# Kernel optimization log

Measured on AMD Instinct MI355X. Metric: run time of the kernel, lower is better.

The kernel has to match this reference:

```python
import jax, jax.numpy as jnp
import numpy as np

N, D = 2048, 64
H, W = 128, 128
NEAR, RADIUS_CLIP, BLUR = 0.01, 3.0, 0.3
A_MIN, A_MAX = 1.0 / 255.0, 0.999


def setup_inputs():
    key = jax.random.key(0)
    k = jax.random.split(key, 6)
    xy = jax.random.uniform(k[0], (N, 2), minval=-1.2, maxval=1.2)
    zz = jax.random.uniform(k[1], (N, 1), minval=3.0, maxval=5.0)
    means = jnp.concatenate([xy, zz], axis=1).astype(jnp.float32)
    quats = jax.random.normal(k[2], (N, 4), dtype=jnp.float32)
    scales = jax.random.normal(k[3], (N, 3), dtype=jnp.float32) * 0.3 - 2.2  # log-scales
    opacities = jax.random.normal(k[4], (N,), dtype=jnp.float32) * 0.5 + 1.0  # logits
    gs_features = jax.random.normal(k[5], (N, D), dtype=jnp.float32) * 0.5
    c2o = jnp.eye(4, dtype=jnp.float32)
    K = jnp.array([[200.0, 0.0, 64.0], [0.0, 200.0, 64.0], [0.0, 0.0, 1.0]], dtype=jnp.float32)
    return dict(means=means, quats=quats, scales=scales, opacities=opacities,
                gs_features=gs_features, c2o=c2o, K=K, width=W, height=H)


def _quat_to_rot(q):
    q = q / jnp.linalg.norm(q, axis=-1, keepdims=True)
    w, x, y, z = q[:, 0], q[:, 1], q[:, 2], q[:, 3]
    r0 = jnp.stack([1 - 2 * (y * y + z * z), 2 * (x * y - w * z), 2 * (x * z + w * y)], -1)
    r1 = jnp.stack([2 * (x * y + w * z), 1 - 2 * (x * x + z * z), 2 * (y * z - w * x)], -1)
    r2 = jnp.stack([2 * (x * z - w * y), 2 * (y * z + w * x), 1 - 2 * (x * x + y * y)], -1)
    return jnp.stack([r0, r1, r2], -2)  # [N,3,3]


def _rasterize(means, quats, log_scales, opac_logits, colors, viewmat, K, width, height):
    Rv, tv = viewmat[:3, :3], viewmat[:3, 3]
    fx, fy, cx, cy = K[0, 0], K[1, 1], K[0, 2], K[1, 2]
    mc = means @ Rv.T + tv                      # camera-space means [N,3]
    x, y, z = mc[:, 0], mc[:, 1], mc[:, 2]
    # 3D covariance Sigma = R S S^T R^T, rotated into camera frame
    M = _quat_to_rot(quats) * jnp.exp(log_scales)[:, None, :]
    cov_w = M @ jnp.swapaxes(M, 1, 2)           # [N,3,3]
    cov_c = jnp.einsum('ij,njk,lk->nil', Rv, cov_w, Rv)
    # perspective (EWA) Jacobian [N,2,3]
    rz = 1.0 / z
    zero = jnp.zeros_like(z)
    J = jnp.stack([jnp.stack([fx * rz, zero, -fx * x * rz * rz], -1),
                   jnp.stack([zero, fy * rz, -fy * y * rz * rz], -1)], -2)
    cov2d = jnp.einsum('nij,njk,nlk->nil', J, cov_c, J)
    a = cov2d[:, 0, 0] + BLUR
    b = cov2d[:, 0, 1]
    c = cov2d[:, 1, 1] + BLUR
    det = a * c - b * b
    cA, cB, cC = c / det, -b / det, a / det     # conic = inverse 2D covariance
    mx = fx * x * rz + cx
    my = fy * y * rz + cy
    # cull: behind near plane, degenerate, or projected 3-sigma radius below radius_clip
    lam_max = 0.5 * (a + c) + jnp.sqrt(jnp.maximum(0.25 * (a - c) ** 2 + b * b, 1e-12))
    radius = 3.0 * jnp.sqrt(lam_max)
    valid = (z > NEAR) & (det > 0) & (radius > RADIUS_CLIP)
    opac = jax.nn.sigmoid(opac_logits)
    # global front-to-back depth order (single camera)
    order = jnp.argsort(z)
    mx, my, cA, cB, cC = mx[order], my[order], cA[order], cB[order], cC[order]
    opac, valid, colors = opac[order], valid[order], colors[order]
    # per pixel-gaussian evaluation, [H,W,N]
    px = jnp.arange(width, dtype=means.dtype) + 0.5
    py = jnp.arange(height, dtype=means.dtype) + 0.5
    dx = px[None, :, None] - mx[None, None, :]
    dy = py[:, None, None] - my[None, None, :]
    sigma = 0.5 * (cA * dx * dx + cC * dy * dy) + cB * dx * dy
    alpha = jnp.minimum(opac * jnp.exp(-sigma), A_MAX)
    alpha = jnp.where((sigma >= 0) & valid & (alpha >= A_MIN), alpha, 0.0)
    # front-to-back alpha compositing: exclusive transmittance cumprod
    Tcum = jnp.cumprod(1.0 - alpha, axis=-1)
    T_excl = jnp.concatenate([jnp.ones_like(Tcum[..., :1]), Tcum[..., :-1]], axis=-1)
    out = jnp.einsum('hwn,nd->hwd', alpha * T_excl, colors)
    return out[None]  # [1,H,W,D]


def reference(means, quats, scales, opacities, gs_features, c2o, K, width, height):
    viewmat = jnp.linalg.inv(c2o)
    return _rasterize(means, quats, scales, opacities, gs_features, viewmat, K, width, height)
```

## Files before the change

kernel.cpp:

```cpp
#include <hip/hip_runtime.h>

constexpr int NG  = 2048;
constexpr int DF  = 64;
constexpr int IW  = 128;
constexpr int IH  = 128;

#define P_NEAR 0.01f
#define P_BLUR 0.3f
#define P_AMIN (1.0f/255.0f)
#define P_AMAX 0.999f

__device__ inline void invert4x4(const float* m, float* inv) {
    inv[0]  =  m[5]*m[10]*m[15] - m[5]*m[11]*m[14] - m[9]*m[6]*m[15] + m[9]*m[7]*m[14] + m[13]*m[6]*m[11] - m[13]*m[7]*m[10];
    inv[4]  = -m[4]*m[10]*m[15] + m[4]*m[11]*m[14] + m[8]*m[6]*m[15] - m[8]*m[7]*m[14] - m[12]*m[6]*m[11] + m[12]*m[7]*m[10];
    inv[8]  =  m[4]*m[9]*m[15]  - m[4]*m[11]*m[13] - m[8]*m[5]*m[15] + m[8]*m[7]*m[13] + m[12]*m[5]*m[11] - m[12]*m[7]*m[9];
    inv[12] = -m[4]*m[9]*m[14]  + m[4]*m[10]*m[13] + m[8]*m[5]*m[14] - m[8]*m[6]*m[13] - m[12]*m[5]*m[10] + m[12]*m[6]*m[9];
    inv[1]  = -m[1]*m[10]*m[15] + m[1]*m[11]*m[14] + m[9]*m[2]*m[15] - m[9]*m[3]*m[14] - m[13]*m[2]*m[11] + m[13]*m[3]*m[10];
    inv[5]  =  m[0]*m[10]*m[15] - m[0]*m[11]*m[14] - m[8]*m[2]*m[15] + m[8]*m[3]*m[14] + m[12]*m[2]*m[11] - m[12]*m[3]*m[10];
    inv[9]  = -m[0]*m[9]*m[15]  + m[0]*m[11]*m[13] + m[8]*m[1]*m[15] - m[8]*m[3]*m[13] - m[12]*m[1]*m[11] + m[12]*m[3]*m[9];
    inv[13] =  m[0]*m[9]*m[14]  - m[0]*m[10]*m[13] - m[8]*m[1]*m[14] + m[8]*m[2]*m[13] + m[12]*m[1]*m[10] - m[12]*m[2]*m[9];
    inv[2]  =  m[1]*m[6]*m[15]  - m[1]*m[7]*m[14]  - m[5]*m[2]*m[15] + m[5]*m[3]*m[14] + m[13]*m[2]*m[7]  - m[13]*m[3]*m[6];
    inv[6]  = -m[0]*m[6]*m[15]  + m[0]*m[7]*m[14]  + m[4]*m[2]*m[15] - m[4]*m[3]*m[14] - m[12]*m[2]*m[7]  + m[12]*m[3]*m[6];
    inv[10] =  m[0]*m[5]*m[15]  - m[0]*m[7]*m[13]  - m[4]*m[1]*m[15] + m[4]*m[3]*m[13] + m[12]*m[1]*m[7]  - m[12]*m[3]*m[5];
    inv[14] = -m[0]*m[5]*m[14]  + m[0]*m[6]*m[13]  + m[4]*m[1]*m[14] - m[4]*m[2]*m[13] - m[12]*m[1]*m[6]  + m[12]*m[2]*m[5];
    inv[3]  = -m[1]*m[6]*m[11]  + m[1]*m[7]*m[10]  + m[5]*m[2]*m[11] - m[5]*m[3]*m[10] - m[9]*m[2]*m[7]   + m[9]*m[3]*m[6];
    inv[7]  =  m[0]*m[6]*m[11]  - m[0]*m[7]*m[10]  - m[4]*m[2]*m[11] + m[4]*m[3]*m[10] + m[8]*m[2]*m[7]   - m[8]*m[3]*m[6];
    inv[11] = -m[0]*m[5]*m[11]  + m[0]*m[7]*m[9]   + m[4]*m[1]*m[11] - m[4]*m[3]*m[9]  - m[8]*m[1]*m[7]   + m[8]*m[3]*m[5];
    inv[15] =  m[0]*m[5]*m[10]  - m[0]*m[6]*m[9]   - m[4]*m[1]*m[10] + m[4]*m[2]*m[9]  + m[8]*m[1]*m[6]   - m[8]*m[2]*m[5];
    float det = m[0]*inv[0] + m[1]*inv[4] + m[2]*inv[8] + m[3]*inv[12];
    det = 1.0f / det;
    #pragma unroll
    for (int i = 0; i < 16; ++i) inv[i] *= det;
}

constexpr int NZ  = 8;
constexpr int RB  = 1024;
constexpr int CAP = 1024;

constexpr int L_T    = 0;
constexpr int L_CNT  = 512;
constexpr int L_SIDX = 528;
constexpr int L_OVL  = L_SIDX + CAP;
constexpr int L_PRM  = L_OVL;
constexpr int L_KEYS = L_PRM + CAP * 8;
constexpr int L_ACC  = L_OVL;
constexpr int ACC_ST = 66;
constexpr int L_TOTAL = L_OVL + NZ * 64 * ACC_ST;

__global__ __launch_bounds__(RB, 4) void fused_render_kernel(
    const float* __restrict__ means,  const float* __restrict__ quats,
    const float* __restrict__ scales, const float* __restrict__ opac_logits,
    const float* __restrict__ colors, const float* __restrict__ c2o,
    const float* __restrict__ Kmat,   float* __restrict__ out)
{
    extern __shared__ float lds[];
    int*                cnt  = (int*)(lds + L_CNT);
    int*                sidx = (int*)(lds + L_SIDX);
    unsigned long long* keys = (unsigned long long*)(lds + L_KEYS);
    float4*             prm4 = (float4*)(lds + L_PRM);

    const int tid  = threadIdx.x;
    const int lane = tid & 63;
    const int wv16 = tid >> 6;
    const int sz   = wv16 >> 1;
    const int hh   = wv16 & 1;
    const int tile = blockIdx.x;
    const int tx = (tile & 15) * 8;
    const int ty = (tile >> 4) * 8;
    const float px = tx + (lane & 7) + 0.5f;
    const float py = ty + (lane >> 3) + 0.5f;
    const float cxt = tx + 4.0f, cyt = ty + 4.0f;

    if (tid == 0) *cnt = 0;
    __syncthreads();

    {
        float inv[16];
        {
            float m[16];
            #pragma unroll
            for (int t = 0; t < 16; ++t) m[t] = c2o[t];
            invert4x4(m, inv);
        }
        const float fx = Kmat[0], fy = Kmat[4], cx = Kmat[2], cy = Kmat[5];

        #pragma unroll
        for (int c = 0; c < NG / RB; ++c) {
            const int g = c * RB + tid;
            float mx = means[g*3+0], my = means[g*3+1], mz = means[g*3+2];
            float X = inv[0]*mx + inv[1]*my + inv[2]*mz  + inv[3];
            float Y = inv[4]*mx + inv[5]*my + inv[6]*mz  + inv[7];
            float Z = inv[8]*mx + inv[9]*my + inv[10]*mz + inv[11];

            float qw = quats[g*4+0], qx = quats[g*4+1], qy = quats[g*4+2], qz = quats[g*4+3];
            float qn = rsqrtf(qw*qw + qx*qx + qy*qy + qz*qz);
            qw *= qn; qx *= qn; qy *= qn; qz *= qn;
            float R00 = 1.f - 2.f*(qy*qy + qz*qz), R01 = 2.f*(qx*qy - qw*qz), R02 = 2.f*(qx*qz + qw*qy);
            float R10 = 2.f*(qx*qy + qw*qz), R11 = 1.f - 2.f*(qx*qx + qz*qz), R12 = 2.f*(qy*qz - qw*qx);
            float R20 = 2.f*(qx*qz - qw*qy), R21 = 2.f*(qy*qz + qw*qx), R22 = 1.f - 2.f*(qx*qx + qy*qy);

            float s0 = expf(scales[g*3+0]), s1 = expf(scales[g*3+1]), s2 = expf(scales[g*3+2]);
            float M00 = R00*s0, M01 = R01*s1, M02 = R02*s2;
            float M10 = R10*s0, M11 = R11*s1, M12 = R12*s2;
            float M20 = R20*s0, M21 = R21*s1, M22 = R22*s2;

            float V00 = M00*M00 + M01*M01 + M02*M02;
            float V01 = M00*M10 + M01*M11 + M02*M12;
            float V02 = M00*M20 + M01*M21 + M02*M22;
            float V11 = M10*M10 + M11*M11 + M12*M12;
            float V12 = M10*M20 + M11*M21 + M12*M22;
            float V22 = M20*M20 + M21*M21 + M22*M22;

            float Rv[3][3] = {{inv[0],inv[1],inv[2]},{inv[4],inv[5],inv[6]},{inv[8],inv[9],inv[10]}};
            float Vm[3][3] = {{V00,V01,V02},{V01,V11,V12},{V02,V12,V22}};
            float Tm[3][3], C[3][3];
            #pragma unroll
            for (int r = 0; r < 3; ++r)
                #pragma unroll
                for (int cc = 0; cc < 3; ++cc)
                    Tm[r][cc] = Rv[r][0]*Vm[0][cc] + Rv[r][1]*Vm[1][cc] + Rv[r][2]*Vm[2][cc];
            #pragma unroll
            for (int r = 0; r < 3; ++r)
                #pragma unroll
                for (int cc = 0; cc < 3; ++cc)
                    C[r][cc] = Tm[r][0]*Rv[cc][0] + Tm[r][1]*Rv[cc][1] + Tm[r][2]*Rv[cc][2];

            float rz = 1.0f / Z;
            float j00 = fx*rz, j02 = -fx*X*rz*rz;
            float j11 = fy*rz, j12 = -fy*Y*rz*rz;

            float c00 = j00*j00*C[0][0] + 2.f*j00*j02*C[0][2] + j02*j02*C[2][2];
            float c01 = j00*j11*C[0][1] + j00*j12*C[0][2] + j02*j11*C[1][2] + j02*j12*C[2][2];
            float c11 = j11*j11*C[1][1] + 2.f*j11*j12*C[1][2] + j12*j12*C[2][2];

            float a = c00 + P_BLUR;
            float b = c01;
            float cc_ = c11 + P_BLUR;
            float det = a*cc_ - b*b;

            float pmx = fx*X*rz + cx;
            float pmy = fy*Y*rz + cy;

            float lam = 0.5f*(a + cc_) + sqrtf(fmaxf(0.25f*(a - cc_)*(a - cc_) + b*b, 1e-12f));
            float radius = 3.0f * sqrtf(lam);
            bool valid = (Z > P_NEAR) && (det > 0.0f) && (radius > 3.0f);

            float op = 1.0f / (1.0f + expf(-opac_logits[g]));

            bool sel = false;
            float cA = 0.f, cB = 0.f, cC2 = 0.f;
            if (valid) {
                float rdet = 1.0f / det;
                cA = cc_ * rdet; cB = -b * rdet; cC2 = a * rdet;
                float smax = logf(255.0f * op);
                if (smax > 0.f) {
                    float rx = sqrtf(2.f * a   * smax) * 1.0001f + 1e-3f;
                    float ry = sqrtf(2.f * cc_ * smax) * 1.0001f + 1e-3f;
                    sel = (fabsf(pmx - cxt) <= rx + 3.5f) && (fabsf(pmy - cyt) <= ry + 3.5f);
                }
            }

            unsigned long long m = __ballot(sel);
            int wbase = 0;
            if (lane == 0 && m) wbase = atomicAdd(cnt, (int)__popcll(m));
            wbase = __shfl(wbase, 0);
            if (sel) {
                int pos = wbase + (int)__popcll(m & ((1ull << lane) - 1ull));
                if (pos < CAP) {
                    prm4[pos*2]   = make_float4(pmx, pmy, cA, cB);
                    prm4[pos*2+1] = make_float4(cC2, op, __int_as_float(g), 0.f);
                    keys[pos] = ((unsigned long long)__float_as_uint(Z) << 32) | (unsigned)g;
                }
            }
        }
    }
    __syncthreads();
    int L = *cnt;
    if (L > CAP) L = CAP;

    {
        int padL = (L + 1) & ~1;
        if (tid < padL - L) keys[L + tid] = ~0ull;
        __syncthreads();
        const ulonglong2* k2 = (const ulonglong2*)keys;
        if (tid < L) {
            unsigned long long kk = keys[tid];
            int rank = 0;
            #pragma unroll 2
            for (int c = 0; c < padL / 2; ++c) {
                ulonglong2 q = k2[c];
                rank += (q.x < kk) + (q.y < kk);
            }
            sidx[rank] = tid;
        }
    }
    __syncthreads();

    float acc[32];
    #pragma unroll
    for (int f = 0; f < 32; ++f) acc[f] = 0.f;
    float T = 1.0f;

    {
        const int r0 = (sz * L) >> 3;
        const int r1 = ((sz + 1) * L) >> 3;
        const float4* cph = (const float4*)colors + hh * 8;
        if (r1 > r0) {
            int k = sidx[r0];
            float4 e0 = prm4[k*2], e1 = prm4[k*2+1];
            for (int r = r0; r < r1; ++r) {
                int kn = (r + 1 < r1) ? sidx[r + 1] : k;
                float4 n0 = prm4[kn*2], n1 = prm4[kn*2+1];

                float dx = px - e0.x, dy = py - e0.y;
                float sig = 0.5f*(e0.z*dx*dx + e1.x*dy*dy) + e0.w*dx*dy;
                float al = fminf(e1.y * __expf(-sig), P_AMAX);
                al = (sig >= 0.f && al >= P_AMIN) ? al : 0.f;

                if (__ballot(al > 0.f)) {
                    float wv = T * al;
                    const float4* crow = cph + (size_t)(unsigned)__float_as_int(e1.z) * 16;
                    #pragma unroll
                    for (int q = 0; q < 8; ++q) {
                        float4 cv = crow[q];
                        acc[4*q+0] = fmaf(wv, cv.x, acc[4*q+0]);
                        acc[4*q+1] = fmaf(wv, cv.y, acc[4*q+1]);
                        acc[4*q+2] = fmaf(wv, cv.z, acc[4*q+2]);
                        acc[4*q+3] = fmaf(wv, cv.w, acc[4*q+3]);
                    }
                    T *= (1.f - al);
                    if (!__ballot(T >= 1e-6f)) break;
                }
                e0 = n0; e1 = n1; k = kn;
            }
        }
    }

    if (hh == 0) lds[L_T + sz*64 + lane] = T;
    __syncthreads();
    {
        float* ab = lds + L_ACC + (size_t)(sz * 64 + lane) * ACC_ST + hh * 32;
        #pragma unroll
        for (int q = 0; q < 16; ++q)
            *(float2*)(ab + 2*q) = make_float2(acc[2*q], acc[2*q+1]);
    }
    __syncthreads();

    {
        int p  = tid >> 4;
        int f0 = (tid & 15) * 4;
        float r0, r1, r2, r3;
        const float* ab = lds + L_ACC + (size_t)((NZ-1)*64 + p) * ACC_ST + f0;
        { float2 u = *(const float2*)ab, v = *(const float2*)(ab + 2);
          r0 = u.x; r1 = u.y; r2 = v.x; r3 = v.y; }
        #pragma unroll
        for (int s = NZ - 2; s >= 0; --s) {
            float Ts = lds[L_T + s*64 + p];
            const float* as_ = lds + L_ACC + (size_t)(s*64 + p) * ACC_ST + f0;
            float2 u = *(const float2*)as_, v = *(const float2*)(as_ + 2);
            r0 = fmaf(Ts, r0, u.x); r1 = fmaf(Ts, r1, u.y);
            r2 = fmaf(Ts, r2, v.x); r3 = fmaf(Ts, r3, v.y);
        }
        int pyg = ty + (p >> 3), pxg = tx + (p & 7);
        float* op_ = out + (size_t)(pyg * IW + pxg) * DF + f0;
        *(float4*)op_ = make_float4(r0, r1, r2, r3);
    }
}

constexpr int ZSL    = 8;
constexpr int NSEG   = 2;
constexpr int NFB    = 2;
constexpr int RTH    = 512;
constexpr int NTILES = 256;
constexpr int EST    = 12;

constexpr size_t WS_SA   = 0;
constexpr size_t WS_SB   = WS_SA   + NG*4;
constexpr size_t WS_SC   = WS_SB   + NG*4;
constexpr size_t WS_SG   = WS_SC   + NG*4;
constexpr size_t WS_T0   = WS_SG   + NG;
constexpr size_t WS_ACC1 = WS_T0   + NTILES*64;
constexpr size_t WS_TCNT = WS_ACC1 + (size_t)NTILES*64*DF;
constexpr size_t WS_TPRM = WS_TCNT + NTILES;
constexpr size_t WS_TOTAL= WS_TPRM + (size_t)NTILES*CAP*8;

__global__ __launch_bounds__(512) void prep_sort_kernel(
    const float* __restrict__ means,  const float* __restrict__ quats,
    const float* __restrict__ scales, const float* __restrict__ opac_logits,
    const float* __restrict__ c2o,    const float* __restrict__ Kmat,
    float* __restrict__ ws)
{
    __shared__ __align__(16) unsigned zlds[NG];
    __shared__ int cnt[8][64];
    const int tid  = threadIdx.x;
    const int lane = tid & 63;
    const int part = tid >> 6;
    const int b    = blockIdx.x;
    const int gown = b * 64 + lane;

    float inv[16];
    {
        float m[16];
        #pragma unroll
        for (int t = 0; t < 16; ++t) m[t] = c2o[t];
        invert4x4(m, inv);
    }
    const float fx = Kmat[0], fy = Kmat[4], cx = Kmat[2], cy = Kmat[5];

    #pragma unroll
    for (int u = 0; u < NG/512; ++u) {
        const int g = u*512 + tid;
        float mx = means[g*3+0], my = means[g*3+1], mz = means[g*3+2];
        float Z = inv[8]*mx + inv[9]*my + inv[10]*mz + inv[11];
        zlds[g] = __float_as_uint(Z);
    }

    float4 A = make_float4(0.f,0.f,0.f,0.f);
    float4 B = make_float4(0.f,0.f,-1e9f,-1e9f);
    if (part == 0) {
        const int g = gown;
        float mx = means[g*3+0], my = means[g*3+1], mz = means[g*3+2];
        float X = inv[0]*mx + inv[1]*my + inv[2]*mz  + inv[3];
        float Y = inv[4]*mx + inv[5]*my + inv[6]*mz  + inv[7];
        float Z = inv[8]*mx + inv[9]*my + inv[10]*mz + inv[11];

        float qw = quats[g*4+0], qx = quats[g*4+1], qy = quats[g*4+2], qz = quats[g*4+3];
        float qn = rsqrtf(qw*qw + qx*qx + qy*qy + qz*qz);
        qw *= qn; qx *= qn; qy *= qn; qz *= qn;
        float R00 = 1.f - 2.f*(qy*qy + qz*qz), R01 = 2.f*(qx*qy - qw*qz), R02 = 2.f*(qx*qz + qw*qy);
        float R10 = 2.f*(qx*qy + qw*qz), R11 = 1.f - 2.f*(qx*qx + qz*qz), R12 = 2.f*(qy*qz - qw*qx);
        float R20 = 2.f*(qx*qz - qw*qy), R21 = 2.f*(qy*qz + qw*qx), R22 = 1.f - 2.f*(qx*qx + qy*qy);

        float s0 = expf(scales[g*3+0]), s1 = expf(scales[g*3+1]), s2 = expf(scales[g*3+2]);
        float M00 = R00*s0, M01 = R01*s1, M02 = R02*s2;
        float M10 = R10*s0, M11 = R11*s1, M12 = R12*s2;
        float M20 = R20*s0, M21 = R21*s1, M22 = R22*s2;

        float V00 = M00*M00 + M01*M01 + M02*M02;
        float V01 = M00*M10 + M01*M11 + M02*M12;
        float V02 = M00*M20 + M01*M21 + M02*M22;
        float V11 = M10*M10 + M11*M11 + M12*M12;
        float V12 = M10*M20 + M11*M21 + M12*M22;
        float V22 = M20*M20 + M21*M21 + M22*M22;

        float Rv[3][3] = {{inv[0],inv[1],inv[2]},{inv[4],inv[5],inv[6]},{inv[8],inv[9],inv[10]}};
        float Vm[3][3] = {{V00,V01,V02},{V01,V11,V12},{V02,V12,V22}};
        float Tm[3][3], C[3][3];
        #pragma unroll
        for (int r = 0; r < 3; ++r)
            #pragma unroll
            for (int cc = 0; cc < 3; ++cc)
                Tm[r][cc] = Rv[r][0]*Vm[0][cc] + Rv[r][1]*Vm[1][cc] + Rv[r][2]*Vm[2][cc];
        #pragma unroll
        for (int r = 0; r < 3; ++r)
            #pragma unroll
            for (int cc = 0; cc < 3; ++cc)
                C[r][cc] = Tm[r][0]*Rv[cc][0] + Tm[r][1]*Rv[cc][1] + Tm[r][2]*Rv[cc][2];

        float rz = 1.0f / Z;
        float j00 = fx*rz, j02 = -fx*X*rz*rz;
        float j11 = fy*rz, j12 = -fy*Y*rz*rz;

        float c00 = j00*j00*C[0][0] + 2.f*j00*j02*C[0][2] + j02*j02*C[2][2];
        float c01 = j00*j11*C[0][1] + j00*j12*C[0][2] + j02*j11*C[1][2] + j02*j12*C[2][2];
        float c11 = j11*j11*C[1][1] + 2.f*j11*j12*C[1][2] + j12*j12*C[2][2];

        float a = c00 + P_BLUR;
        float bb = c01;
        float cc_ = c11 + P_BLUR;
        float det = a*cc_ - bb*bb;

        float pmx = fx*X*rz + cx;
        float pmy = fy*Y*rz + cy;

        float lam = 0.5f*(a + cc_) + sqrtf(fmaxf(0.25f*(a - cc_)*(a - cc_) + bb*bb, 1e-12f));
        float radius = 3.0f * sqrtf(lam);
        bool valid = (Z > P_NEAR) && (det > 0.0f) && (radius > 3.0f);

        float op = 1.0f / (1.0f + expf(-opac_logits[g]));

        float cA = 0.f, cB = 0.f, cC2 = 0.f, rx = -1e9f, ry = -1e9f;
        if (valid) {
            float rdet = 1.0f / det;
            cA = cc_ * rdet; cB = -bb * rdet; cC2 = a * rdet;
            float smax = logf(255.0f * op);
            if (smax > 0.f) {
                rx = sqrtf(2.f * a   * smax) * 1.0001f + 1e-3f;
                ry = sqrtf(2.f * cc_ * smax) * 1.0001f + 1e-3f;
            }
        }
        A = make_float4(pmx, pmy, cA, cB);
        B = make_float4(cC2, op, rx, ry);
    }
    __syncthreads();

    const unsigned kk = zlds[b*64 + lane];
    const uint4* zl4 = (const uint4*)zlds;
    int c = 0;
    #pragma unroll 4
    for (int i = part*64; i < part*64 + 64; ++i) {
        uint4 q = zl4[i];
        const int j = i * 4;
        c += (q.x < kk || (q.x == kk && j+0 < gown)) ? 1 : 0;
        c += (q.y < kk || (q.y == kk && j+1 < gown)) ? 1 : 0;
        c += (q.z < kk || (q.z == kk && j+2 < gown)) ? 1 : 0;
        c += (q.w < kk || (q.w == kk && j+3 < gown)) ? 1 : 0;
    }
    cnt[part][lane] = c;
    __syncthreads();
    if (part == 0) {
        int rank = 0;
        #pragma unroll
        for (int e = 0; e < 8; ++e) rank += cnt[e][lane];
        ((float4*)(ws + WS_SA))[rank] = A;
        ((float4*)(ws + WS_SB))[rank] = B;
        ((float4*)(ws + WS_SC))[rank] = make_float4(A.x, A.y, B.z, B.w);
        ((int*)  (ws + WS_SG))[rank] = gown;
    }
}

__global__ __launch_bounds__(512) void cull_tile_kernel(float* __restrict__ ws)
{
    __shared__ int s_wcnt[8];
    const int tid  = threadIdx.x;
    const int lane = tid & 63;
    const int w    = tid >> 6;
    const int tile = blockIdx.x;
    const int tx = (tile & 15) * 8, ty = (tile >> 4) * 8;
    const float cxt = tx + 4.0f, cyt = ty + 4.0f;

    const float4* sA = (const float4*)(ws + WS_SA);
    const float4* sB = (const float4*)(ws + WS_SB);
    const float4* sC = (const float4*)(ws + WS_SC);
    const int*    sG = (const int*)  (ws + WS_SG);
    float4* tp = (float4*)(ws + WS_TPRM + (size_t)tile * CAP * 8);

    int Lrun = 0;
    #pragma unroll
    for (int ch = 0; ch < NG/RTH; ++ch) {
        const int j = ch*RTH + tid;
        float4 C = sC[j];
        bool sel = (fabsf(C.x - cxt) <= C.z + 3.5f) && (fabsf(C.y - cyt) <= C.w + 3.5f);
        unsigned long long m = __ballot(sel);
        if (lane == 0) s_wcnt[w] = (int)__popcll(m);
        __syncthreads();
        int pre = 0, tot = 0;
        #pragma unroll
        for (int e = 0; e < 8; ++e) { int cw = s_wcnt[e]; pre += (e < w) ? cw : 0; tot += cw; }
        if (sel) {
            int pos = Lrun + pre + (int)__popcll(m & ((1ull << lane) - 1ull));
            if (pos < CAP) {
                float4 Aa = sA[j], Bb = sB[j];
                tp[pos*2]   = Aa;
                tp[pos*2+1] = make_float4(Bb.x, Bb.y, __int_as_float(sG[j]), 0.f);
            }
        }
        Lrun += tot;
        __syncthreads();
    }
    if (tid == 0) ((int*)(ws + WS_TCNT))[tile] = (Lrun < CAP) ? Lrun : CAP;
}

__global__ __launch_bounds__(RTH) void raster_kernel(
    const float* __restrict__ colors, float* __restrict__ ws,
    float* __restrict__ out)
{
    __shared__ float ureg[CAP*8];
    __shared__ float Tlds[ZSL*64];

    const int tid  = threadIdx.x;
    const int lane = tid & 63;
    const int w    = tid >> 6;
    const int b    = blockIdx.x;
    const int tile = b >> 2;
    const int k    = b & 3;
    const int seg  = k >> 1;
    const int fb   = k & 1;
    const int tx = (tile & 15) * 8, ty = (tile >> 4) * 8;
    const float px = tx + (lane & 7) + 0.5f;
    const float py = ty + (lane >> 3) + 0.5f;

    float4* prm4 = (float4*)ureg;
    const int L = ((const int*)(ws + WS_TCNT))[tile];
    {
        const float4* tp = (const float4*)(ws + WS_TPRM + (size_t)tile * CAP * 8);
        for (int i = tid; i < 2*L; i += RTH) prm4[i] = tp[i];
    }
    __syncthreads();

    float acc[32];
    #pragma unroll
    for (int i = 0; i < 32; ++i) acc[i] = 0.f;
    float T = 1.0f;
    {
        const int v  = seg * ZSL + w;
        const int r0 = (v * L) >> 4;
        const int r1 = ((v + 1) * L) >> 4;
        const float4* cph = (const float4*)colors + fb * 8;
        if (r1 > r0) {
            float4 e0 = prm4[2*r0], e1 = prm4[2*r0+1];
            for (int r = r0; r < r1; ++r) {
                const int gi = __builtin_amdgcn_readfirstlane(__float_as_int(e1.z));
                const float4* crow = cph + (size_t)(unsigned)gi * (DF/4);
                float4 c0 = crow[0], c1 = crow[1], c2 = crow[2], c3 = crow[3];
                float4 c4 = crow[4], c5 = crow[5], c6 = crow[6], c7 = crow[7];

                const int rn = (r + 1 < r1) ? r + 1 : r;
                float4 n0 = prm4[2*rn], n1 = prm4[2*rn+1];

                float dx = px - e0.x, dy = py - e0.y;
                float sig = 0.5f*(e0.z*dx*dx + e1.x*dy*dy) + e0.w*dx*dy;
                float al = fminf(e1.y * __expf(-sig), P_AMAX);
                al = (sig >= 0.f && al >= P_AMIN) ? al : 0.f;

                if (__ballot(al > 0.f)) {
                    float wv = T * al;
                    acc[0]  = fmaf(wv, c0.x, acc[0]);  acc[1]  = fmaf(wv, c0.y, acc[1]);
                    acc[2]  = fmaf(wv, c0.z, acc[2]);  acc[3]  = fmaf(wv, c0.w, acc[3]);
                    acc[4]  = fmaf(wv, c1.x, acc[4]);  acc[5]  = fmaf(wv, c1.y, acc[5]);
                    acc[6]  = fmaf(wv, c1.z, acc[6]);  acc[7]  = fmaf(wv, c1.w, acc[7]);
                    acc[8]  = fmaf(wv, c2.x, acc[8]);  acc[9]  = fmaf(wv, c2.y, acc[9]);
                    acc[10] = fmaf(wv, c2.z, acc[10]); acc[11] = fmaf(wv, c2.w, acc[11]);
                    acc[12] = fmaf(wv, c3.x, acc[12]); acc[13] = fmaf(wv, c3.y, acc[13]);
                    acc[14] = fmaf(wv, c3.z, acc[14]); acc[15] = fmaf(wv, c3.w, acc[15]);
                    acc[16] = fmaf(wv, c4.x, acc[16]); acc[17] = fmaf(wv, c4.y, acc[17]);
                    acc[18] = fmaf(wv, c4.z, acc[18]); acc[19] = fmaf(wv, c4.w, acc[19]);
                    acc[20] = fmaf(wv, c5.x, acc[20]); acc[21] = fmaf(wv, c5.y, acc[21]);
                    acc[22] = fmaf(wv, c5.z, acc[22]); acc[23] = fmaf(wv, c5.w, acc[23]);
                    acc[24] = fmaf(wv, c6.x, acc[24]); acc[25] = fmaf(wv, c6.y, acc[25]);
                    acc[26] = fmaf(wv, c6.z, acc[26]); acc[27] = fmaf(wv, c6.w, acc[27]);
                    acc[28] = fmaf(wv, c7.x, acc[28]); acc[29] = fmaf(wv, c7.y, acc[29]);
                    acc[30] = fmaf(wv, c7.z, acc[30]); acc[31] = fmaf(wv, c7.w, acc[31]);
                    T *= (1.f - al);
                    if (!__ballot(T >= 1e-6f)) break;
                }
                e0 = n0; e1 = n1;
            }
        }
    }

    Tlds[w*64 + lane] = T;
    __syncthreads();

    if (seg == 0 && fb == 0 && tid < 64) {
        float tp = 1.f;
        #pragma unroll
        for (int s = 0; s < ZSL; ++s) tp *= Tlds[s*64 + tid];
        ws[WS_T0 + tile*64 + tid] = tp;
    }

    #pragma unroll
    for (int pass = 0; pass < 8; ++pass) {
        float* ab = ureg + (w*64 + lane) * EST;
        *(float4*)ab = make_float4(acc[pass*4+0], acc[pass*4+1], acc[pass*4+2], acc[pass*4+3]);
        __syncthreads();
        if (tid < 256) {
            const int p = tid >> 2, c = tid & 3;
            float r = ureg[((ZSL-1)*64 + p)*EST + c];
            #pragma unroll
            for (int s = ZSL-2; s >= 0; --s)
                r = fmaf(Tlds[s*64 + p], r, ureg[(s*64 + p)*EST + c]);
            const int pxg = tx + (p & 7), pyg = ty + (p >> 3);
            const int fi = fb*32 + pass*4 + c;
            if (seg == 0) out[(size_t)(pyg*IW + pxg)*DF + fi] = r;
            else          ws[WS_ACC1 + ((size_t)tile*64 + p)*DF + fi] = r;
        }
        __syncthreads();
    }
}

__global__ __launch_bounds__(1024) void combine_kernel(
    float* __restrict__ out, const float* __restrict__ ws)
{
    const int tile = blockIdx.x;
    const int p  = threadIdx.x >> 4;
    const int f0 = (threadIdx.x & 15) * 4;
    const int pxg = (tile & 15)*8 + (p & 7);
    const int pyg = (tile >> 4)*8 + (p >> 3);
    const float T0 = ws[WS_T0 + tile*64 + p];
    const float4 a1 = *(const float4*)(ws + WS_ACC1 + ((size_t)tile*64 + p)*DF + f0);
    float4* o = (float4*)(out + (size_t)(pyg*IW + pxg)*DF + f0);
    float4 v = *o;
    v.x = fmaf(T0, a1.x, v.x);
    v.y = fmaf(T0, a1.y, v.y);
    v.z = fmaf(T0, a1.z, v.z);
    v.w = fmaf(T0, a1.w, v.w);
    *o = v;
}

extern "C" void kernel_launch(void* const* d_in, const int* in_sizes, int n_in,
                              void* d_out, int out_size, void* d_ws, size_t ws_size,
                              hipStream_t stream) {
    const float* means  = (const float*)d_in[0];
    const float* quats  = (const float*)d_in[1];
    const float* scales = (const float*)d_in[2];
    const float* opac   = (const float*)d_in[3];
    const float* colors = (const float*)d_in[4];
    const float* c2o    = (const float*)d_in[5];
    const float* Kmat   = (const float*)d_in[6];
    float* out = (float*)d_out;

    if (ws_size >= WS_TOTAL * sizeof(float)) {
        float* ws = (float*)d_ws;
        prep_sort_kernel   <<<NG/64,              512, 0, stream>>>(means, quats, scales, opac, c2o, Kmat, ws);
        cull_tile_kernel   <<<NTILES,             512, 0, stream>>>(ws);
        raster_kernel      <<<NTILES*NSEG*NFB,    RTH, 0, stream>>>(colors, ws, out);
        combine_kernel     <<<NTILES,             1024,0, stream>>>(out, ws);
    } else {
        (void)hipFuncSetAttribute((const void*)fused_render_kernel,
                                  hipFuncAttributeMaxDynamicSharedMemorySize,
                                  L_TOTAL * 4);
        fused_render_kernel<<<IH*IW/64, RB, L_TOTAL*4, stream>>>(
            means, quats, scales, opac, colors, c2o, Kmat, out);
    }
}
```

Before: 110.2 us.

## Fuse tile culling into raster kernel and drop depth-segment split with combine pass

Moves per-tile culling into the raster kernel so each block builds its gaussian list directly in LDS instead of writing it to and rereading it from the workspace. It also removes the two-segment depth split, so each block covers the whole depth range with 8 wave slices, and drops the combine kernel along with the T0/ACC1 workspace buffers. This cuts the pipeline from four launches to two and removes intermediate global traffic. In exchange there are half as many raster blocks (512 instead of 1024), each wave walks twice as many gaussians, and the culling scan is repeated for both feature halves of a tile.

```diff
diff --git a/kernel.cpp b/kernel.cpp
--- a/kernel.cpp
+++ b/kernel.cpp
@@ -268,7 +268,6 @@
 }
 
 constexpr int ZSL    = 8;
-constexpr int NSEG   = 2;
 constexpr int NFB    = 2;
 constexpr int RTH    = 512;
 constexpr int NTILES = 256;
@@ -278,11 +277,7 @@
 constexpr size_t WS_SB   = WS_SA   + NG*4;
 constexpr size_t WS_SC   = WS_SB   + NG*4;
 constexpr size_t WS_SG   = WS_SC   + NG*4;
-constexpr size_t WS_T0   = WS_SG   + NG;
-constexpr size_t WS_ACC1 = WS_T0   + NTILES*64;
-constexpr size_t WS_TCNT = WS_ACC1 + (size_t)NTILES*64*DF;
-constexpr size_t WS_TPRM = WS_TCNT + NTILES;
-constexpr size_t WS_TOTAL= WS_TPRM + (size_t)NTILES*CAP*8;
+constexpr size_t WS_TOTAL= WS_SG   + NG;
 
 __global__ __launch_bounds__(512) void prep_sort_kernel(
     const float* __restrict__ means,  const float* __restrict__ quats,
@@ -419,21 +414,30 @@
     }
 }
 
-__global__ __launch_bounds__(512) void cull_tile_kernel(float* __restrict__ ws)
+__global__ __launch_bounds__(RTH) void raster_kernel(
+    const float* __restrict__ colors, float* __restrict__ ws,
+    float* __restrict__ out)
 {
-    __shared__ int s_wcnt[8];
+    __shared__ float ureg[CAP*8];
+    __shared__ float Tlds[ZSL*64];
+    __shared__ int   s_wcnt[8];
+
     const int tid  = threadIdx.x;
     const int lane = tid & 63;
     const int w    = tid >> 6;
-    const int tile = blockIdx.x;
+    const int b    = blockIdx.x;
+    const int tile = b >> 1;
+    const int fb   = b & 1;
     const int tx = (tile & 15) * 8, ty = (tile >> 4) * 8;
+    const float px = tx + (lane & 7) + 0.5f;
+    const float py = ty + (lane >> 3) + 0.5f;
     const float cxt = tx + 4.0f, cyt = ty + 4.0f;
 
+    float4* prm4 = (float4*)ureg;
     const float4* sA = (const float4*)(ws + WS_SA);
     const float4* sB = (const float4*)(ws + WS_SB);
     const float4* sC = (const float4*)(ws + WS_SC);
     const int*    sG = (const int*)  (ws + WS_SG);
-    float4* tp = (float4*)(ws + WS_TPRM + (size_t)tile * CAP * 8);
 
     int Lrun = 0;
     #pragma unroll
@@ -451,51 +455,22 @@
             int pos = Lrun + pre + (int)__popcll(m & ((1ull << lane) - 1ull));
             if (pos < CAP) {
                 float4 Aa = sA[j], Bb = sB[j];
-                tp[pos*2]   = Aa;
-                tp[pos*2+1] = make_float4(Bb.x, Bb.y, __int_as_float(sG[j]), 0.f);
+                prm4[pos*2]   = Aa;
+                prm4[pos*2+1] = make_float4(Bb.x, Bb.y, __int_as_float(sG[j]), 0.f);
             }
         }
         Lrun += tot;
         __syncthreads();
     }
-    if (tid == 0) ((int*)(ws + WS_TCNT))[tile] = (Lrun < CAP) ? Lrun : CAP;
-}
-
-__global__ __launch_bounds__(RTH) void raster_kernel(
-    const float* __restrict__ colors, float* __restrict__ ws,
-    float* __restrict__ out)
-{
-    __shared__ float ureg[CAP*8];
-    __shared__ float Tlds[ZSL*64];
-
-    const int tid  = threadIdx.x;
-    const int lane = tid & 63;
-    const int w    = tid >> 6;
-    const int b    = blockIdx.x;
-    const int tile = b >> 2;
-    const int k    = b & 3;
-    const int seg  = k >> 1;
-    const int fb   = k & 1;
-    const int tx = (tile & 15) * 8, ty = (tile >> 4) * 8;
-    const float px = tx + (lane & 7) + 0.5f;
-    const float py = ty + (lane >> 3) + 0.5f;
-
-    float4* prm4 = (float4*)ureg;
-    const int L = ((const int*)(ws + WS_TCNT))[tile];
-    {
-        const float4* tp = (const float4*)(ws + WS_TPRM + (size_t)tile * CAP * 8);
-        for (int i = tid; i < 2*L; i += RTH) prm4[i] = tp[i];
-    }
-    __syncthreads();
+    const int L = (Lrun < CAP) ? Lrun : CAP;
 
     float acc[32];
     #pragma unroll
     for (int i = 0; i < 32; ++i) acc[i] = 0.f;
     float T = 1.0f;
     {
-        const int v  = seg * ZSL + w;
-        const int r0 = (v * L) >> 4;
-        const int r1 = ((v + 1) * L) >> 4;
+        const int r0 = (w * L) >> 3;
+        const int r1 = ((w + 1) * L) >> 3;
         const float4* cph = (const float4*)colors + fb * 8;
         if (r1 > r0) {
             float4 e0 = prm4[2*r0], e1 = prm4[2*r0+1];
@@ -542,13 +517,6 @@
     Tlds[w*64 + lane] = T;
     __syncthreads();
 
-    if (seg == 0 && fb == 0 && tid < 64) {
-        float tp = 1.f;
-        #pragma unroll
-        for (int s = 0; s < ZSL; ++s) tp *= Tlds[s*64 + tid];
-        ws[WS_T0 + tile*64 + tid] = tp;
-    }
-
     #pragma unroll
     for (int pass = 0; pass < 8; ++pass) {
         float* ab = ureg + (w*64 + lane) * EST;
@@ -562,30 +530,10 @@
                 r = fmaf(Tlds[s*64 + p], r, ureg[(s*64 + p)*EST + c]);
             const int pxg = tx + (p & 7), pyg = ty + (p >> 3);
             const int fi = fb*32 + pass*4 + c;
-            if (seg == 0) out[(size_t)(pyg*IW + pxg)*DF + fi] = r;
-            else          ws[WS_ACC1 + ((size_t)tile*64 + p)*DF + fi] = r;
+            out[(size_t)(pyg*IW + pxg)*DF + fi] = r;
         }
         __syncthreads();
     }
-}
-
-__global__ __launch_bounds__(1024) void combine_kernel(
-    float* __restrict__ out, const float* __restrict__ ws)
-{
-    const int tile = blockIdx.x;
-    const int p  = threadIdx.x >> 4;
-    const int f0 = (threadIdx.x & 15) * 4;
-    const int pxg = (tile & 15)*8 + (p & 7);
-    const int pyg = (tile >> 4)*8 + (p >> 3);
-    const float T0 = ws[WS_T0 + tile*64 + p];
-    const float4 a1 = *(const float4*)(ws + WS_ACC1 + ((size_t)tile*64 + p)*DF + f0);
-    float4* o = (float4*)(out + (size_t)(pyg*IW + pxg)*DF + f0);
-    float4 v = *o;
-    v.x = fmaf(T0, a1.x, v.x);
-    v.y = fmaf(T0, a1.y, v.y);
-    v.z = fmaf(T0, a1.z, v.z);
-    v.w = fmaf(T0, a1.w, v.w);
-    *o = v;
 }
 
 extern "C" void kernel_launch(void* const* d_in, const int* in_sizes, int n_in,
@@ -602,10 +550,8 @@
 
     if (ws_size >= WS_TOTAL * sizeof(float)) {
         float* ws = (float*)d_ws;
-        prep_sort_kernel   <<<NG/64,              512, 0, stream>>>(means, quats, scales, opac, c2o, Kmat, ws);
-        cull_tile_kernel   <<<NTILES,             512, 0, stream>>>(ws);
-        raster_kernel      <<<NTILES*NSEG*NFB,    RTH, 0, stream>>>(colors, ws, out);
-        combine_kernel     <<<NTILES,             1024,0, stream>>>(out, ws);
+        prep_sort_kernel<<<NG/64,        512, 0, stream>>>(means, quats, scales, opac, c2o, Kmat, ws);
+        raster_kernel   <<<NTILES*NFB,   RTH, 0, stream>>>(colors, ws, out);
     } else {
         (void)hipFuncSetAttribute((const void*)fused_render_kernel,
                                   hipFuncAttributeMaxDynamicSharedMemorySize,
```

Result: faster. 104.2 us (-5.4%).
